# Optimization experiments

Measured on AMD Instinct MI355X. Metric: run time of the kernel, lower is better.

Reference implementation:

```python
import jax, jax.numpy as jnp
import numpy as np

EMB = 256
ENT_NUM = 100000
REL_NUM = 2000
B = 512


def setup_inputs() -> dict:
    key = jax.random.key(0)
    ks = jax.random.split(key, 10)
    s = 0.02
    return {
        "left_child": jax.random.normal(ks[0], (B, 3, EMB), jnp.float32),
        "right_child": jax.random.normal(ks[1], (B, 3, EMB), jnp.float32),
        "query": jax.random.normal(ks[2], (B, 3, EMB), jnp.float32),
        "ent_emb": jax.random.normal(ks[3], (ENT_NUM, EMB), jnp.float32) * s,
        "rel_emb": jax.random.normal(ks[4], (REL_NUM, EMB), jnp.float32) * s,
        "W_left": jax.random.normal(ks[5], (EMB, EMB), jnp.float32) * s,
        "b_left": jnp.zeros((EMB,), jnp.float32),
        "W_right": jax.random.normal(ks[6], (EMB, EMB), jnp.float32) * s,
        "b_right": jnp.zeros((EMB,), jnp.float32),
        "W_ent": jax.random.normal(ks[7], (EMB, 3 * EMB), jnp.float32) * s,
        "b_ent": jnp.zeros((EMB,), jnp.float32),
    }


def _attend(q, table):
    # q: [B, E], table: [N, E]. Fused form of expand*mul*sum + softmax + expand*mul*sum.
    logits = q @ table.T                     # [B, N]
    probs = jax.nn.softmax(logits, axis=1)   # [B, N]
    return probs @ table                     # [B, E]


def reference(left_child, right_child, query, ent_emb, rel_emb,
              W_left, b_left, W_right, b_right, W_ent, b_ent):
    q1 = query[:, 1, :]
    left_rel = q1 @ W_left.T + b_left
    right_rel = q1 @ W_right.T + b_right
    # cat(query[:,0], query[:,1], query[:,2]) along dim 1 == reshape
    q_cat = query.reshape(query.shape[0], 3 * EMB)
    q_ent = q_cat @ W_ent.T + b_ent

    o_ent = _attend(q_ent, ent_emb)
    o_left_r = _attend(left_rel, rel_emb)
    o_right_r = _attend(right_rel, rel_emb)

    new_left = jnp.stack([left_child[:, 0, :], o_left_r, o_ent], axis=1)
    new_right = jnp.stack([o_ent, o_right_r, right_child[:, 2, :]], axis=1)
    return (new_left, new_right)
```

## Files before the change

### kernel.cpp

```cpp
#include <hip/hip_runtime.h>
#include <hip/hip_bf16.h>
#include <math.h>

typedef __bf16 bf16;
typedef unsigned short u16;
typedef unsigned int u32;
typedef unsigned long long u64;
typedef long long i64;
typedef unsigned char u8;
typedef __attribute__((ext_vector_type(8))) __bf16 bf16x8;
typedef __attribute__((ext_vector_type(16))) float f32x16;
typedef __attribute__((ext_vector_type(8))) int i32x8;
typedef __attribute__((address_space(1))) void gvoid;
typedef __attribute__((address_space(3))) void svoid;

#define ENT_N 100000
#define REL_N 2000
#define ENT_CH 120
#define REL_CH 4

#define NPREPM 1536
#define NITEMS 6380
#define NCONVB 1792
#define NCOPY  256

static __device__ __forceinline__ i32x8 mk8(uint4 a, uint4 b) {
    i32x8 r;
    r[0] = (int)a.x; r[1] = (int)a.y; r[2] = (int)a.z; r[3] = (int)a.w;
    r[4] = (int)b.x; r[5] = (int)b.y; r[6] = (int)b.z; r[7] = (int)b.w;
    return r;
}

template<int KLEN>
static __device__ __forceinline__ void prep_tile(
    const float* __restrict__ query, const float* __restrict__ W,
    const float* __restrict__ bias, int b0, int rowbase, int qwoff,
    bf16* __restrict__ outBf, u8* __restrict__ out8, float* smem)
{
    const int t = threadIdx.x;
    float* qs = smem;
    float* Wl = smem + 4 * KLEN;

#pragma unroll
    for (int i = 0; i < 4 * KLEN / 256; ++i) {
        const int l = t + 256 * i;
        const int r = l / KLEN, k = l % KLEN;
        qs[l] = query[(size_t)(b0 + r) * 768 + qwoff + k];
    }

    const int j = t & 63, r = t >> 6;
    float acc = 0.f;
    const float* wbase = W + (size_t)rowbase * KLEN;

    for (int c = 0; c < KLEN / 32; ++c) {
        __syncthreads();
#pragma unroll
        for (int p = 0; p < 2; ++p) {
            const int idx = t + p * 256;
            const int row = idx >> 3, kq = idx & 7;
            const float4 v = *(const float4*)(wbase + (size_t)row * KLEN + c * 32 + kq * 4);
            float* d = Wl + row * 33 + kq * 4;
            d[0] = v.x; d[1] = v.y; d[2] = v.z; d[3] = v.w;
        }
        __syncthreads();
        const float* wr = Wl + j * 33;
        const float* qr = qs + r * KLEN + c * 32;
#pragma unroll
        for (int k = 0; k < 32; ++k) acc += wr[k] * qr[k];
    }
    acc += bias[rowbase + j];

    const size_t o = (size_t)(b0 + r) * 256 + rowbase + j;
    outBf[o] = (bf16)acc;
    out8[o] = (u8)__builtin_amdgcn_cvt_pk_fp8_f32(acc, acc, 0, false);
}

__global__ __launch_bounds__(256) void prep_conv(
    const float* __restrict__ query,
    const float* __restrict__ W_left, const float* __restrict__ b_left,
    const float* __restrict__ W_right, const float* __restrict__ b_right,
    const float* __restrict__ W_ent, const float* __restrict__ b_ent,
    const float* __restrict__ lc, const float* __restrict__ rc,
    bf16* __restrict__ qe, bf16* __restrict__ ql, bf16* __restrict__ qr,
    u8* __restrict__ qe8, u8* __restrict__ ql8, u8* __restrict__ qr8,
    float* __restrict__ out,
    const float* __restrict__ entF, const float* __restrict__ relF,
    u8* __restrict__ entT, u8* __restrict__ entB,
    u8* __restrict__ relT, u8* __restrict__ relB,
    int nconv)
{
    __shared__ float smem[5184];
    const int blk = blockIdx.x;
    const int t = threadIdx.x;

    if (blk >= nconv && blk < nconv + NPREPM) {
        const int pb = blk - nconv;
        const int rg = pb / 12, jt = pb % 12;
        const int b0 = rg * 4;
        const int proj = jt >> 2, rowbase = (jt & 3) * 64;
        if (proj == 0)
            prep_tile<768>(query, W_ent, b_ent, b0, rowbase, 0, qe, qe8, smem);
        else if (proj == 1)
            prep_tile<256>(query, W_left, b_left, b0, rowbase, 256, ql, ql8, smem);
        else
            prep_tile<256>(query, W_right, b_right, b0, rowbase, 256, qr, qr8, smem);
        return;
    }
    if (blk >= nconv + NPREPM) {
        const int idx = (blk - nconv - NPREPM) * 256 + t;
        if (idx < 32768) {
            const int q = idx >> 6, e4 = idx & 63;
            float4 v = *(const float4*)(lc + (size_t)q * 768 + e4 * 4);
            *(float4*)(out + (size_t)q * 768 + e4 * 4) = v;
        } else {
            const int j = idx - 32768;
            const int q = j >> 6, e4 = j & 63;
            float4 v = *(const float4*)(rc + (size_t)q * 768 + 512 + e4 * 4);
            *(float4*)(out + (size_t)393216 + q * 768 + 512 + e4 * 4) = v;
        }
        return;
    }

    float* tile = smem;
    const int eg = t & 7, rowb = t >> 3;

    float4 A0, B0, A1, B1;

    auto cissue = [&](int it) {
        const int x = it >> 2, y = it & 3;
        const float* in; int R, g;
        if (x < 1563) { in = entF; R = ENT_N; g = x; }
        else          { in = relF; R = REL_N; g = x - 1563; }
        const int r0 = g * 64, e0 = y * 64;
        const int ra = r0 + rowb, rb = r0 + rowb + 32;
        if (ra < R) {
            const float* s0 = in + (size_t)ra * 256 + e0 + eg * 8;
            A0 = *(const float4*)s0; B0 = *(const float4*)(s0 + 4);
        } else { A0 = make_float4(0.f, 0.f, 0.f, 0.f); B0 = A0; }
        if (rb < R) {
            const float* s1 = in + (size_t)rb * 256 + e0 + eg * 8;
            A1 = *(const float4*)s1; B1 = *(const float4*)(s1 + 4);
        } else { A1 = make_float4(0.f, 0.f, 0.f, 0.f); B1 = A1; }
    };

    auto cemit = [&](int it) {
        const int x = it >> 2, y = it & 3;
        u8* oT; u8* oB; int g;
        if (x < 1563) { oT = entT; oB = entB; g = x; }
        else          { oT = relT; oB = relB; g = x - 1563; }
        {
            const int n2 = t >> 2, piece = t & 3;
            const int sub = n2 >> 5, nn = n2 & 31;
            const int kbk = piece >> 1, jh = piece & 1;
            const float* src = tile + n2 * 65 + kbk * 32 + jh * 16;
            u32 xx; uint4 o;
            xx = __builtin_amdgcn_cvt_pk_fp8_f32(src[0], src[1], 0, false);
            o.x = __builtin_amdgcn_cvt_pk_fp8_f32(src[2], src[3], xx, true);
            xx = __builtin_amdgcn_cvt_pk_fp8_f32(src[4], src[5], 0, false);
            o.y = __builtin_amdgcn_cvt_pk_fp8_f32(src[6], src[7], xx, true);
            xx = __builtin_amdgcn_cvt_pk_fp8_f32(src[8], src[9], 0, false);
            o.z = __builtin_amdgcn_cvt_pk_fp8_f32(src[10], src[11], xx, true);
            xx = __builtin_amdgcn_cvt_pk_fp8_f32(src[12], src[13], 0, false);
            o.w = __builtin_amdgcn_cvt_pk_fp8_f32(src[14], src[15], xx, true);
            *(uint4*)(oB + (size_t)g * 16384 + sub * 8192 +
                      (size_t)y * 2048 + kbk * 1024 + nn * 32 + jh * 16) = o;
        }
        {
            const int etl = t >> 7, kbv = (t >> 6) & 1;
            const int nv = (t >> 1) & 31, jh = t & 1;
            const int colL = etl * 32 + nv;
            float v[16];
#pragma unroll
            for (int i = 0; i < 16; ++i) {
                const int row = jh * 32 + (i & 3) + 8 * (i >> 2) + 4 * kbv;
                v[i] = tile[row * 65 + colL];
            }
            u32 xx; uint4 o;
            xx = __builtin_amdgcn_cvt_pk_fp8_f32(v[0], v[1], 0, false);
            o.x = __builtin_amdgcn_cvt_pk_fp8_f32(v[2], v[3], xx, true);
            xx = __builtin_amdgcn_cvt_pk_fp8_f32(v[4], v[5], 0, false);
            o.y = __builtin_amdgcn_cvt_pk_fp8_f32(v[6], v[7], xx, true);
            xx = __builtin_amdgcn_cvt_pk_fp8_f32(v[8], v[9], 0, false);
            o.z = __builtin_amdgcn_cvt_pk_fp8_f32(v[10], v[11], xx, true);
            xx = __builtin_amdgcn_cvt_pk_fp8_f32(v[12], v[13], 0, false);
            o.w = __builtin_amdgcn_cvt_pk_fp8_f32(v[14], v[15], xx, true);
            *(uint4*)(oT + (size_t)g * 16384 +
                      (size_t)(y * 2 + etl) * 2048 +
                      kbv * 1024 + nv * 32 + jh * 16) = o;
        }
    };

    int it = blk;
    cissue(it);
    while (it < NITEMS) {
        const int nxt = it + NCONVB;
        __syncthreads();
        {
            float* d0 = tile + rowb * 65 + eg * 8;
            d0[0] = A0.x; d0[1] = A0.y; d0[2] = A0.z; d0[3] = A0.w;
            d0[4] = B0.x; d0[5] = B0.y; d0[6] = B0.z; d0[7] = B0.w;
            float* d1 = tile + (rowb + 32) * 65 + eg * 8;
            d1[0] = A1.x; d1[1] = A1.y; d1[2] = A1.z; d1[3] = A1.w;
            d1[4] = B1.x; d1[5] = B1.y; d1[6] = B1.z; d1[7] = B1.w;
        }
        if (nxt < NITEMS) cissue(nxt);
        __syncthreads();
        cemit(it);
        it = nxt;
    }
}

__global__ __launch_bounds__(256, 2) void flash10(
    const u8* __restrict__ qeP, const u8* __restrict__ qlP,
    const u8* __restrict__ qrP,
    const u8* __restrict__ entB, const u8* __restrict__ relB,
    const u8* __restrict__ entT, const u8* __restrict__ relT,
    float* __restrict__ entL, float* __restrict__ relLL,
    float* __restrict__ relLR,
    u16* __restrict__ entO, u16* __restrict__ relOL, u16* __restrict__ relOR)
{
    const int tid = threadIdx.x;
    const int w = tid >> 6;
    const int lane = tid & 63;
    const int n = lane & 31;
    const int kb = lane >> 5;

    int qt, c, stride, nt, Nrows;
    const u8* qbf; const u8* tabB; const u8* tabT;
    float* pL; u16* pO;
    {
        const int id = blockIdx.x;
        if (id < 480) {
            qt = id / 120; c = id % 120;
            stride = 120; nt = (c < 3) ? 14 : 13;
            Nrows = ENT_N;
            qbf = qeP; tabB = entB; tabT = entT; pL = entL; pO = entO;
        } else {
            const int r = id - 480;
            qt = (r >> 2) & 3; c = r & 3;
            stride = 4; nt = 8;
            Nrows = REL_N;
            tabB = relB; tabT = relT;
            if (r < 16) { qbf = qlP; pL = relLL; pO = relOL; }
            else        { qbf = qrP; pL = relLR; pO = relOR; }
        }
    }
    const int q0 = qt * 128;
    const int qw = q0 + w * 32;

    __shared__ __align__(16) u8 lds[65536];
    u16* lds16 = (u16*)lds;

    const u8* qrow = qbf + (size_t)(qw + n) * 256;
    i32x8 qf[4];
#pragma unroll
    for (int kc = 0; kc < 4; ++kc) {
        uint4 a = *(const uint4*)(qrow + kc * 64 + kb * 32);
        uint4 b = *(const uint4*)(qrow + kc * 64 + kb * 32 + 16);
        qf[kc] = mk8(a, b);
    }

    f32x16 acc[8];
#pragma unroll
    for (int et = 0; et < 8; ++et)
#pragma unroll
        for (int i = 0; i < 16; ++i) acc[et][i] = 0.f;
    float l_run = 0.f;

    auto stage = [&](int buf, int g) {
        u8* sK = lds + buf * 32768;
        u8* sV = sK + 16384;
        const u8* ksrc = tabB + (size_t)g * 16384 + w * 4096 + (size_t)lane * 16;
        const u8* vsrc = tabT + (size_t)g * 16384 + w * 4096 + (size_t)lane * 16;
#pragma unroll
        for (int o = 0; o < 4096; o += 1024) {
            __builtin_amdgcn_global_load_lds((gvoid*)(ksrc + o),
                                             (svoid*)(sK + w * 4096 + o), 16, 0, 0);
            __builtin_amdgcn_global_load_lds((gvoid*)(vsrc + o),
                                             (svoid*)(sV + w * 4096 + o), 16, 0, 0);
        }
    };

    int rt = c;
    stage(0, rt);
    __syncthreads();

    for (int k = 0; k < nt; ++k) {
        if (k + 1 < nt) stage((k + 1) & 1, rt + stride);

        const u8* sK = lds + (k & 1) * 32768;
        const u8* sV = sK + 16384;
        const int gr = rt * 64;

        f32x16 L0, L1;
#pragma unroll
        for (int i = 0; i < 16; ++i) { L0[i] = 0.f; L1[i] = 0.f; }
        const u8* kbase = sK + kb * 1024 + n * 32;
#pragma unroll
        for (int kc = 0; kc < 4; ++kc) {
            uint4 a0 = *(const uint4*)(kbase + kc * 2048);
            uint4 a1 = *(const uint4*)(kbase + kc * 2048 + 16);
            L0 = __builtin_amdgcn_mfma_scale_f32_32x32x64_f8f6f4(
                mk8(a0, a1), qf[kc], L0, 0, 0, 0, 0x7f7f7f7f, 0, 0x7f7f7f7f);
            uint4 b0 = *(const uint4*)(kbase + 8192 + kc * 2048);
            uint4 b1 = *(const uint4*)(kbase + 8192 + kc * 2048 + 16);
            L1 = __builtin_amdgcn_mfma_scale_f32_32x32x64_f8f6f4(
                mk8(b0, b1), qf[kc], L1, 0, 0, 0, 0x7f7f7f7f, 0, 0x7f7f7f7f);
        }
        if (gr + 64 > Nrows) {
#pragma unroll
            for (int r = 0; r < 16; ++r) {
                const int row = (r & 3) + 8 * (r >> 2) + 4 * kb;
                if (gr + row >= Nrows)      L0[r] = -1e30f;
                if (gr + 32 + row >= Nrows) L1[r] = -1e30f;
            }
        }
        float rs = 0.f;
#pragma unroll
        for (int r = 0; r < 16; ++r) {
            const float p0 = __expf(L0[r]); L0[r] = p0; rs += p0;
            const float p1 = __expf(L1[r]); L1[r] = p1; rs += p1;
        }
        rs += __shfl_xor(rs, 32);
        l_run += rs;
        u32 p[8];
#pragma unroll
        for (int i = 0; i < 4; ++i) {
            u32 x = __builtin_amdgcn_cvt_pk_fp8_f32(L0[i * 4 + 0], L0[i * 4 + 1], 0, false);
            p[i] = __builtin_amdgcn_cvt_pk_fp8_f32(L0[i * 4 + 2], L0[i * 4 + 3], x, true);
            u32 y = __builtin_amdgcn_cvt_pk_fp8_f32(L1[i * 4 + 0], L1[i * 4 + 1], 0, false);
            p[i + 4] = __builtin_amdgcn_cvt_pk_fp8_f32(L1[i * 4 + 2], L1[i * 4 + 3], y, true);
        }
        uint4 pa; pa.x = p[0]; pa.y = p[1]; pa.z = p[2]; pa.w = p[3];
        uint4 pb; pb.x = p[4]; pb.y = p[5]; pb.z = p[6]; pb.w = p[7];
        const i32x8 bv = mk8(pa, pb);
        const u8* vbase = sV + kb * 1024 + n * 32;
#pragma unroll
        for (int et = 0; et < 8; ++et) {
            uint4 v0 = *(const uint4*)(vbase + et * 2048);
            uint4 v1 = *(const uint4*)(vbase + et * 2048 + 16);
            acc[et] = __builtin_amdgcn_mfma_scale_f32_32x32x64_f8f6f4(
                mk8(v0, v1), bv, acc[et], 0, 0, 0, 0x7f7f7f7f, 0, 0x7f7f7f7f);
        }
        rt += stride;
        __syncthreads();
    }

    if (lane < 32) pL[(size_t)c * 512 + qw + n] = l_run;

    for (int half = 0; half < 2; ++half) {
        __syncthreads();
        if ((w >> 1) == half) {
            u16* rgn = lds16 + (w & 1) * 8448;
#pragma unroll
            for (int et = 0; et < 8; ++et)
#pragma unroll
                for (int a2 = 0; a2 < 4; ++a2) {
                    bf16 h0 = (bf16)acc[et][a2 * 4 + 0];
                    bf16 h1 = (bf16)acc[et][a2 * 4 + 1];
                    bf16 h2 = (bf16)acc[et][a2 * 4 + 2];
                    bf16 h3 = (bf16)acc[et][a2 * 4 + 3];
                    uint2 pk;
                    pk.x = ((u32)(*(u16*)&h1) << 16) | (u32)(*(u16*)&h0);
                    pk.y = ((u32)(*(u16*)&h3) << 16) | (u32)(*(u16*)&h2);
                    *(uint2*)(rgn + n * 264 + et * 32 + 8 * a2 + 4 * kb) = pk;
                }
        }
        __syncthreads();
#pragma unroll
        for (int rg = 0; rg < 2; ++rg) {
            const int qt2 = q0 + (half * 2 + rg) * 32;
            const u16* src = lds16 + rg * 8448;
            const int qq = tid >> 3, e0 = (tid & 7) * 32;
#pragma unroll
            for (int i = 0; i < 4; ++i) {
                const u16* sp = src + qq * 264 + e0 + i * 8;
                uint2 a = *(const uint2*)(sp);
                uint2 b = *(const uint2*)(sp + 4);
                uint4 wv; wv.x = a.x; wv.y = a.y; wv.z = b.x; wv.w = b.y;
                *(uint4*)(pO + ((size_t)c * 512 + qt2 + qq) * 256 + e0 + i * 8) = wv;
            }
        }
    }
}

__global__ __launch_bounds__(256) void combine_all(
    const u16* __restrict__ entO, const float* __restrict__ entL,
    const u16* __restrict__ relOL, const float* __restrict__ relLL,
    const u16* __restrict__ relOR, const float* __restrict__ relLR,
    float* __restrict__ out)
{
    const u16* pO; const float* pl; int CH, baseA, baseB;
    if (blockIdx.y == 0) { pO = entO; pl = entL; CH = ENT_CH; baseA = 512; baseB = 393216; }
    else if (blockIdx.y == 1) { pO = relOL; pl = relLL; CH = REL_CH; baseA = 256; baseB = -1; }
    else { pO = relOR; pl = relLR; CH = REL_CH; baseA = 393472; baseB = -1; }

    const int t = threadIdx.x;
    const int qi = t >> 7;
    const int e0g = (t >> 2) & 31;
    const int seg = t & 3;
    const int q = blockIdx.x * 2 + qi;
    const int e0 = e0g * 8;
    const int cnt = CH >> 2;
    const int cbeg = seg * cnt;

    float s = 0.f;
    float a[8];
#pragma unroll
    for (int k = 0; k < 8; ++k) a[k] = 0.f;
#pragma unroll 6
    for (int c = cbeg; c < cbeg + cnt; ++c) {
        s += pl[(size_t)c * 512 + q];
        const uint4 wv = *(const uint4*)(pO + ((size_t)c * 512 + q) * 256 + e0);
        const u32 ww[4] = {wv.x, wv.y, wv.z, wv.w};
#pragma unroll
        for (int p = 0; p < 4; ++p) {
            a[p * 2]     += __uint_as_float((ww[p] & 0xffffu) << 16);
            a[p * 2 + 1] += __uint_as_float(ww[p] & 0xffff0000u);
        }
    }

    __shared__ float red[2][32][4][11];
    float* slot = red[qi][e0g][seg];
#pragma unroll
    for (int k = 0; k < 8; ++k) slot[k] = a[k];
    slot[8] = s;
    __syncthreads();
    if (seg == 0) {
        float st = 0.f;
        float b[8];
#pragma unroll
        for (int k = 0; k < 8; ++k) b[k] = 0.f;
#pragma unroll
        for (int sgi = 0; sgi < 4; ++sgi) {
            const float* sl = red[qi][e0g][sgi];
            st += sl[8];
#pragma unroll
            for (int k = 0; k < 8; ++k) b[k] += sl[k];
        }
        const float inv = 1.f / st;
#pragma unroll
        for (int k = 0; k < 8; ++k) b[k] *= inv;
        float4 o1 = {b[0], b[1], b[2], b[3]};
        float4 o2 = {b[4], b[5], b[6], b[7]};
        *(float4*)(out + (size_t)baseA + (size_t)q * 768 + e0) = o1;
        *(float4*)(out + (size_t)baseA + (size_t)q * 768 + e0 + 4) = o2;
        if (baseB >= 0) {
            *(float4*)(out + (size_t)baseB + (size_t)q * 768 + e0) = o1;
            *(float4*)(out + (size_t)baseB + (size_t)q * 768 + e0 + 4) = o2;
        }
    }
}

__global__ __launch_bounds__(256) void attend_simple(
    const bf16* __restrict__ qbf, const float* __restrict__ tab, int Nrows,
    float* __restrict__ out, int baseA, int baseB)
{
    const int q = blockIdx.x;
    const int t = threadIdx.x, wave = t >> 6, lane = t & 63;
    float qv[4];
#pragma unroll
    for (int i = 0; i < 4; ++i) qv[i] = (float)qbf[(size_t)q * 256 + lane + 64 * i];
    float m = -INFINITY, l = 0.f, o[4] = {0.f, 0.f, 0.f, 0.f};
    for (int r = wave; r < Nrows; r += 4) {
        const float* row = tab + (size_t)r * 256;
        float d = 0.f;
#pragma unroll
        for (int i = 0; i < 4; ++i) d += qv[i] * row[lane + 64 * i];
#pragma unroll
        for (int s = 32; s; s >>= 1) d += __shfl_xor(d, s);
        const float mn = fmaxf(m, d);
        const float al = __expf(m - mn);
        const float p = __expf(d - mn);
#pragma unroll
        for (int i = 0; i < 4; ++i) o[i] = o[i] * al + p * row[lane + 64 * i];
        l = l * al + p; m = mn;
    }
    __shared__ float sm[4], sl[4], so[4][256];
    if (lane == 0) { sm[wave] = m; sl[wave] = l; }
#pragma unroll
    for (int i = 0; i < 4; ++i) so[wave][lane + 64 * i] = o[i];
    __syncthreads();
    const float M = fmaxf(fmaxf(sm[0], sm[1]), fmaxf(sm[2], sm[3]));
    const float w0 = __expf(sm[0] - M), w1 = __expf(sm[1] - M);
    const float w2 = __expf(sm[2] - M), w3 = __expf(sm[3] - M);
    const float L = w0 * sl[0] + w1 * sl[1] + w2 * sl[2] + w3 * sl[3];
    const float a = (w0 * so[0][t] + w1 * so[1][t] + w2 * so[2][t] + w3 * so[3][t]) / L;
    out[(size_t)baseA + (size_t)q * 768 + t] = a;
    if (baseB >= 0) out[(size_t)baseB + (size_t)q * 768 + t] = a;
}

extern "C" void kernel_launch(void* const* d_in, const int* in_sizes, int n_in,
                              void* d_out, int out_size, void* d_ws, size_t ws_size,
                              hipStream_t stream)
{
    const float* left_child  = (const float*)d_in[0];
    const float* right_child = (const float*)d_in[1];
    const float* query       = (const float*)d_in[2];
    const float* ent_emb     = (const float*)d_in[3];
    const float* rel_emb     = (const float*)d_in[4];
    const float* W_left      = (const float*)d_in[5];
    const float* b_left      = (const float*)d_in[6];
    const float* W_right     = (const float*)d_in[7];
    const float* b_right     = (const float*)d_in[8];
    const float* W_ent       = (const float*)d_in[9];
    const float* b_ent       = (const float*)d_in[10];
    float* out = (float*)d_out;
    char* ws = (char*)d_ws;

    bf16* qe_bf = (bf16*)(ws + 0);
    bf16* ql_bf = (bf16*)(ws + 262144);
    bf16* qr_bf = (bf16*)(ws + 524288);
    u8*   qe8   = (u8*)(ws + 786432);
    u8*   ql8   = (u8*)(ws + 917504);
    u8*   qr8   = (u8*)(ws + 1048576);
    u8*   entT8 = (u8*)(ws + 1179648);
    u8*   relT8 = (u8*)(ws + 26787840);
    u8*   entB8 = (u8*)(ws + 27312128);
    u8*   relB8 = (u8*)(ws + 52920320);
    float* entL = (float*)(ws + 53444608);
    u16*  entO  = (u16*)(ws + 53690368);
    float* relLL = (float*)(ws + 85147648);
    float* relLR = (float*)(ws + 85155840);
    u16*  relOL = (u16*)(ws + 85164032);
    u16*  relOR = (u16*)(ws + 86212608);
    const size_t WS_FULL = 87261184;
    const size_t WS_FALLBACK = 786432;

    if (ws_size >= WS_FULL) {
        prep_conv<<<dim3(NCONVB + NPREPM + NCOPY), dim3(256), 0, stream>>>(
            query, W_left, b_left, W_right, b_right, W_ent, b_ent,
            left_child, right_child, qe_bf, ql_bf, qr_bf, qe8, ql8, qr8, out,
            ent_emb, rel_emb, entT8, entB8, relT8, relB8, NCONVB);
        flash10<<<dim3(512), dim3(256), 0, stream>>>(
            qe8, ql8, qr8, entB8, relB8, entT8, relT8,
            entL, relLL, relLR, entO, relOL, relOR);
        combine_all<<<dim3(256, 3), dim3(256), 0, stream>>>(
            entO, entL, relOL, relLL, relOR, relLR, out);
    } else if (ws_size >= WS_FALLBACK) {
        prep_conv<<<dim3(NPREPM + NCOPY), dim3(256), 0, stream>>>(
            query, W_left, b_left, W_right, b_right, W_ent, b_ent,
            left_child, right_child, qe_bf, ql_bf, qr_bf, qe8, ql8, qr8, out,
            ent_emb, rel_emb, (u8*)ws, (u8*)ws, (u8*)ws, (u8*)ws, 0);
        attend_simple<<<dim3(512), dim3(256), 0, stream>>>(qe_bf, ent_emb, ENT_N, out, 512, 393216);
        attend_simple<<<dim3(512), dim3(256), 0, stream>>>(ql_bf, rel_emb, REL_N, out, 256, -1);
        attend_simple<<<dim3(512), dim3(256), 0, stream>>>(qr_bf, rel_emb, REL_N, out, 393472, -1);
    }
    (void)in_sizes; (void)n_in; (void)out_size;
}
```

Baseline: 252.1 us.

## Fuse prep, flash attention and combine into one persistent kernel with grid barriers

Replaces the three launches (prep/convert, flash attention, combine) with one persistent kernel of 512 blocks. The stages are separated by atomic-counter grid barriers, and the table conversion loop prefetches the next item's loads. It also double-buffers the weight tiles in the projection prep. This removes launch gaps and tail idle time between kernels, at the cost of a memset, spin-wait barriers that rely on all 512 blocks being co-resident, and lower per-stage occupancy flexibility.

```diff
diff --git a/kernel.cpp b/kernel.cpp
--- a/kernel.cpp
+++ b/kernel.cpp
@@ -8,7 +8,6 @@
 typedef unsigned long long u64;
 typedef long long i64;
 typedef unsigned char u8;
-typedef __attribute__((ext_vector_type(8))) __bf16 bf16x8;
 typedef __attribute__((ext_vector_type(16))) float f32x16;
 typedef __attribute__((ext_vector_type(8))) int i32x8;
 typedef __attribute__((address_space(1))) void gvoid;
@@ -21,14 +20,26 @@
 
 #define NPREPM 1536
 #define NITEMS 6380
-#define NCONVB 1792
 #define NCOPY  256
+#define NBLK   512
 
 static __device__ __forceinline__ i32x8 mk8(uint4 a, uint4 b) {
     i32x8 r;
     r[0] = (int)a.x; r[1] = (int)a.y; r[2] = (int)a.z; r[3] = (int)a.w;
     r[4] = (int)b.x; r[5] = (int)b.y; r[6] = (int)b.z; r[7] = (int)b.w;
     return r;
+}
+
+static __device__ __forceinline__ void grid_barrier(u32* cnt) {
+    __syncthreads();
+    if (threadIdx.x == 0) {
+        __threadfence();
+        atomicAdd(cnt, 1u);
+        while (atomicAdd(cnt, 0u) < (u32)NBLK)
+            __builtin_amdgcn_s_sleep(2);
+        __threadfence();
+    }
+    __syncthreads();
 }
 
 template<int KLEN>
@@ -49,24 +60,33 @@
     }
 
     const int j = t & 63, r = t >> 6;
+    const int srow = t >> 3, skq = t & 7;
+    const float* wbase = W + (size_t)rowbase * KLEN;
+
+    float4 v0, v1;
+    auto wload = [&](int c) {
+        v0 = *(const float4*)(wbase + (size_t)srow * KLEN + c * 32 + skq * 4);
+        v1 = *(const float4*)(wbase + (size_t)(srow + 32) * KLEN + c * 32 + skq * 4);
+    };
+    auto wstore = [&](float* dst) {
+        float* d0 = dst + srow * 33 + skq * 4;
+        d0[0] = v0.x; d0[1] = v0.y; d0[2] = v0.z; d0[3] = v0.w;
+        float* d1 = dst + (srow + 32) * 33 + skq * 4;
+        d1[0] = v1.x; d1[1] = v1.y; d1[2] = v1.z; d1[3] = v1.w;
+    };
+
     float acc = 0.f;
-    const float* wbase = W + (size_t)rowbase * KLEN;
-
-    for (int c = 0; c < KLEN / 32; ++c) {
+    wload(0);
+    wstore(Wl);
+    constexpr int NC = KLEN / 32;
+    for (int c = 0; c < NC; ++c) {
+        if (c + 1 < NC) wload(c + 1);
         __syncthreads();
-#pragma unroll
-        for (int p = 0; p < 2; ++p) {
-            const int idx = t + p * 256;
-            const int row = idx >> 3, kq = idx & 7;
-            const float4 v = *(const float4*)(wbase + (size_t)row * KLEN + c * 32 + kq * 4);
-            float* d = Wl + row * 33 + kq * 4;
-            d[0] = v.x; d[1] = v.y; d[2] = v.z; d[3] = v.w;
-        }
-        __syncthreads();
-        const float* wr = Wl + j * 33;
+        const float* wr = Wl + (c & 1) * 2112 + j * 33;
         const float* qr = qs + r * KLEN + c * 32;
 #pragma unroll
         for (int k = 0; k < 32; ++k) acc += wr[k] * qr[k];
+        if (c + 1 < NC) wstore(Wl + ((c + 1) & 1) * 2112);
     }
     acc += bias[rowbase + j];
 
@@ -75,7 +95,372 @@
     out8[o] = (u8)__builtin_amdgcn_cvt_pk_fp8_f32(acc, acc, 0, false);
 }
 
-__global__ __launch_bounds__(256) void prep_conv(
+struct FusedArgs {
+    const float *query, *W_left, *b_left, *W_right, *b_right, *W_ent, *b_ent;
+    const float *lc, *rc, *entF, *relF;
+    bf16 *qe, *ql, *qr;
+    u8 *qe8, *ql8, *qr8;
+    u8 *entT, *entB, *relT, *relB;
+    float *entL, *relLL, *relLR;
+    u16 *entO, *relOL, *relOR;
+    float *out;
+    u32 *cnt0, *cnt1;
+};
+
+__global__ __launch_bounds__(256, 2) void fused_all(FusedArgs A)
+{
+    const int t = threadIdx.x;
+    const int tid = t;
+    const int w = tid >> 6;
+    const int lane = tid & 63;
+    const int n = lane & 31;
+    const int kb = lane >> 5;
+
+    __shared__ __align__(16) u8 lds[65536];
+
+    {
+        float* tile = (float*)lds;
+        const int eg = t & 7, rowb = t >> 3;
+        float4 A0, B0, A1, B1;
+        int pf = -1;
+
+        auto cissue = [&](int it) {
+            const int x = it >> 2, y = it & 3;
+            const float* in; int R, g;
+            if (x < 1563) { in = A.entF; R = ENT_N; g = x; }
+            else          { in = A.relF; R = REL_N; g = x - 1563; }
+            const int r0 = g * 64, e0 = y * 64;
+            const int ra = r0 + rowb, rb = r0 + rowb + 32;
+            if (ra < R) {
+                const float* s0 = in + (size_t)ra * 256 + e0 + eg * 8;
+                A0 = *(const float4*)s0; B0 = *(const float4*)(s0 + 4);
+            } else { A0 = make_float4(0.f, 0.f, 0.f, 0.f); B0 = A0; }
+            if (rb < R) {
+                const float* s1 = in + (size_t)rb * 256 + e0 + eg * 8;
+                A1 = *(const float4*)s1; B1 = *(const float4*)(s1 + 4);
+            } else { A1 = make_float4(0.f, 0.f, 0.f, 0.f); B1 = A1; }
+        };
+        auto cemit = [&](int it) {
+            const int x = it >> 2, y = it & 3;
+            u8* oT; u8* oB; int g;
+            if (x < 1563) { oT = A.entT; oB = A.entB; g = x; }
+            else          { oT = A.relT; oB = A.relB; g = x - 1563; }
+            {
+                const int n2 = t >> 2, piece = t & 3;
+                const int sub = n2 >> 5, nn = n2 & 31;
+                const int kbk = piece >> 1, jh = piece & 1;
+                const float* src = tile + n2 * 65 + kbk * 32 + jh * 16;
+                u32 xx; uint4 o;
+                xx = __builtin_amdgcn_cvt_pk_fp8_f32(src[0], src[1], 0, false);
+                o.x = __builtin_amdgcn_cvt_pk_fp8_f32(src[2], src[3], xx, true);
+                xx = __builtin_amdgcn_cvt_pk_fp8_f32(src[4], src[5], 0, false);
+                o.y = __builtin_amdgcn_cvt_pk_fp8_f32(src[6], src[7], xx, true);
+                xx = __builtin_amdgcn_cvt_pk_fp8_f32(src[8], src[9], 0, false);
+                o.z = __builtin_amdgcn_cvt_pk_fp8_f32(src[10], src[11], xx, true);
+                xx = __builtin_amdgcn_cvt_pk_fp8_f32(src[12], src[13], 0, false);
+                o.w = __builtin_amdgcn_cvt_pk_fp8_f32(src[14], src[15], xx, true);
+                *(uint4*)(oB + (size_t)g * 16384 + sub * 8192 +
+                          (size_t)y * 2048 + kbk * 1024 + nn * 32 + jh * 16) = o;
+            }
+            {
+                const int etl = t >> 7, kbv = (t >> 6) & 1;
+                const int nv = (t >> 1) & 31, jh = t & 1;
+                const int colL = etl * 32 + nv;
+                float v[16];
+#pragma unroll
+                for (int i = 0; i < 16; ++i) {
+                    const int row = jh * 32 + (i & 3) + 8 * (i >> 2) + 4 * kbv;
+                    v[i] = tile[row * 65 + colL];
+                }
+                u32 xx; uint4 o;
+                xx = __builtin_amdgcn_cvt_pk_fp8_f32(v[0], v[1], 0, false);
+                o.x = __builtin_amdgcn_cvt_pk_fp8_f32(v[2], v[3], xx, true);
+                xx = __builtin_amdgcn_cvt_pk_fp8_f32(v[4], v[5], 0, false);
+                o.y = __builtin_amdgcn_cvt_pk_fp8_f32(v[6], v[7], xx, true);
+                xx = __builtin_amdgcn_cvt_pk_fp8_f32(v[8], v[9], 0, false);
+                o.z = __builtin_amdgcn_cvt_pk_fp8_f32(v[10], v[11], xx, true);
+                xx = __builtin_amdgcn_cvt_pk_fp8_f32(v[12], v[13], 0, false);
+                o.w = __builtin_amdgcn_cvt_pk_fp8_f32(v[14], v[15], xx, true);
+                *(uint4*)(oT + (size_t)g * 16384 +
+                          (size_t)(y * 2 + etl) * 2048 +
+                          kbv * 1024 + nv * 32 + jh * 16) = o;
+            }
+        };
+
+        for (int it = blockIdx.x; it < NITEMS + NPREPM + NCOPY; it += NBLK) {
+            if (it < NITEMS) {
+                if (pf != it) cissue(it);
+                __syncthreads();
+                float* d0 = tile + rowb * 65 + eg * 8;
+                d0[0] = A0.x; d0[1] = A0.y; d0[2] = A0.z; d0[3] = A0.w;
+                d0[4] = B0.x; d0[5] = B0.y; d0[6] = B0.z; d0[7] = B0.w;
+                float* d1 = tile + (rowb + 32) * 65 + eg * 8;
+                d1[0] = A1.x; d1[1] = A1.y; d1[2] = A1.z; d1[3] = A1.w;
+                d1[4] = B1.x; d1[5] = B1.y; d1[6] = B1.z; d1[7] = B1.w;
+                const int nxt = it + NBLK;
+                if (nxt < NITEMS) { cissue(nxt); pf = nxt; }
+                __syncthreads();
+                cemit(it);
+            } else if (it < NITEMS + NPREPM) {
+                __syncthreads();
+                const int pb = it - NITEMS;
+                const int rg = pb / 12, jt = pb % 12;
+                const int b0 = rg * 4;
+                const int proj = jt >> 2, rowbase = (jt & 3) * 64;
+                if (proj == 0)
+                    prep_tile<768>(A.query, A.W_ent, A.b_ent, b0, rowbase, 0,
+                                   A.qe, A.qe8, (float*)lds);
+                else if (proj == 1)
+                    prep_tile<256>(A.query, A.W_left, A.b_left, b0, rowbase, 256,
+                                   A.ql, A.ql8, (float*)lds);
+                else
+                    prep_tile<256>(A.query, A.W_right, A.b_right, b0, rowbase, 256,
+                                   A.qr, A.qr8, (float*)lds);
+            } else {
+                const int idx = (it - NITEMS - NPREPM) * 256 + t;
+                if (idx < 32768) {
+                    const int q = idx >> 6, e4 = idx & 63;
+                    float4 v = *(const float4*)(A.lc + (size_t)q * 768 + e4 * 4);
+                    *(float4*)(A.out + (size_t)q * 768 + e4 * 4) = v;
+                } else {
+                    const int j2 = idx - 32768;
+                    const int q = j2 >> 6, e4 = j2 & 63;
+                    float4 v = *(const float4*)(A.rc + (size_t)q * 768 + 512 + e4 * 4);
+                    *(float4*)(A.out + (size_t)393216 + q * 768 + 512 + e4 * 4) = v;
+                }
+            }
+        }
+    }
+    grid_barrier(A.cnt0);
+
+    {
+        u16* lds16 = (u16*)lds;
+        int qt, c, stride, nt, Nrows;
+        const u8* qbf; const u8* tabB; const u8* tabT;
+        float* pL; u16* pO;
+        {
+            const int id = blockIdx.x;
+            if (id < 480) {
+                qt = id / 120; c = id % 120;
+                stride = 120; nt = (c < 3) ? 14 : 13;
+                Nrows = ENT_N;
+                qbf = A.qe8; tabB = A.entB; tabT = A.entT; pL = A.entL; pO = A.entO;
+            } else {
+                const int r = id - 480;
+                qt = (r >> 2) & 3; c = r & 3;
+                stride = 4; nt = 8;
+                Nrows = REL_N;
+                tabB = A.relB; tabT = A.relT;
+                if (r < 16) { qbf = A.ql8; pL = A.relLL; pO = A.relOL; }
+                else        { qbf = A.qr8; pL = A.relLR; pO = A.relOR; }
+            }
+        }
+        const int q0 = qt * 128;
+        const int qw = q0 + w * 32;
+
+        const u8* qrow = qbf + (size_t)(qw + n) * 256;
+        i32x8 qf[4];
+#pragma unroll
+        for (int kc = 0; kc < 4; ++kc) {
+            uint4 a = *(const uint4*)(qrow + kc * 64 + kb * 32);
+            uint4 b = *(const uint4*)(qrow + kc * 64 + kb * 32 + 16);
+            qf[kc] = mk8(a, b);
+        }
+
+        f32x16 acc[8];
+#pragma unroll
+        for (int et = 0; et < 8; ++et)
+#pragma unroll
+            for (int i = 0; i < 16; ++i) acc[et][i] = 0.f;
+        float l_run = 0.f;
+
+        auto stage = [&](int buf, int g2) {
+            u8* sK = lds + buf * 32768;
+            u8* sV = sK + 16384;
+            const u8* ksrc = tabB + (size_t)g2 * 16384 + w * 4096 + (size_t)lane * 16;
+            const u8* vsrc = tabT + (size_t)g2 * 16384 + w * 4096 + (size_t)lane * 16;
+#pragma unroll
+            for (int o = 0; o < 4096; o += 1024) {
+                __builtin_amdgcn_global_load_lds((gvoid*)(ksrc + o),
+                                                 (svoid*)(sK + w * 4096 + o), 16, 0, 0);
+                __builtin_amdgcn_global_load_lds((gvoid*)(vsrc + o),
+                                                 (svoid*)(sV + w * 4096 + o), 16, 0, 0);
+            }
+        };
+
+        int rt = c;
+        stage(0, rt);
+        __syncthreads();
+
+        for (int k = 0; k < nt; ++k) {
+            if (k + 1 < nt) stage((k + 1) & 1, rt + stride);
+
+            const u8* sK = lds + (k & 1) * 32768;
+            const u8* sV = sK + 16384;
+            const int gr = rt * 64;
+
+            f32x16 L0, L1;
+#pragma unroll
+            for (int i = 0; i < 16; ++i) { L0[i] = 0.f; L1[i] = 0.f; }
+            const u8* kbase = sK + kb * 1024 + n * 32;
+#pragma unroll
+            for (int kc = 0; kc < 4; ++kc) {
+                uint4 a0 = *(const uint4*)(kbase + kc * 2048);
+                uint4 a1 = *(const uint4*)(kbase + kc * 2048 + 16);
+                L0 = __builtin_amdgcn_mfma_scale_f32_32x32x64_f8f6f4(
+                    mk8(a0, a1), qf[kc], L0, 0, 0, 0, 0x7f7f7f7f, 0, 0x7f7f7f7f);
+                uint4 b0 = *(const uint4*)(kbase + 8192 + kc * 2048);
+                uint4 b1 = *(const uint4*)(kbase + 8192 + kc * 2048 + 16);
+                L1 = __builtin_amdgcn_mfma_scale_f32_32x32x64_f8f6f4(
+                    mk8(b0, b1), qf[kc], L1, 0, 0, 0, 0x7f7f7f7f, 0, 0x7f7f7f7f);
+            }
+            if (gr + 64 > Nrows) {
+#pragma unroll
+                for (int r = 0; r < 16; ++r) {
+                    const int row = (r & 3) + 8 * (r >> 2) + 4 * kb;
+                    if (gr + row >= Nrows)      L0[r] = -1e30f;
+                    if (gr + 32 + row >= Nrows) L1[r] = -1e30f;
+                }
+            }
+            float rs = 0.f;
+#pragma unroll
+            for (int r = 0; r < 16; ++r) {
+                const float p0 = __expf(L0[r]); L0[r] = p0; rs += p0;
+                const float p1 = __expf(L1[r]); L1[r] = p1; rs += p1;
+            }
+            rs += __shfl_xor(rs, 32);
+            l_run += rs;
+            u32 p[8];
+#pragma unroll
+            for (int i = 0; i < 4; ++i) {
+                u32 x = __builtin_amdgcn_cvt_pk_fp8_f32(L0[i * 4 + 0], L0[i * 4 + 1], 0, false);
+                p[i] = __builtin_amdgcn_cvt_pk_fp8_f32(L0[i * 4 + 2], L0[i * 4 + 3], x, true);
+                u32 y = __builtin_amdgcn_cvt_pk_fp8_f32(L1[i * 4 + 0], L1[i * 4 + 1], 0, false);
+                p[i + 4] = __builtin_amdgcn_cvt_pk_fp8_f32(L1[i * 4 + 2], L1[i * 4 + 3], y, true);
+            }
+            uint4 pa; pa.x = p[0]; pa.y = p[1]; pa.z = p[2]; pa.w = p[3];
+            uint4 pb; pb.x = p[4]; pb.y = p[5]; pb.z = p[6]; pb.w = p[7];
+            const i32x8 bv = mk8(pa, pb);
+            const u8* vbase = sV + kb * 1024 + n * 32;
+#pragma unroll
+            for (int et = 0; et < 8; ++et) {
+                uint4 v0 = *(const uint4*)(vbase + et * 2048);
+                uint4 v1 = *(const uint4*)(vbase + et * 2048 + 16);
+                acc[et] = __builtin_amdgcn_mfma_scale_f32_32x32x64_f8f6f4(
+                    mk8(v0, v1), bv, acc[et], 0, 0, 0, 0x7f7f7f7f, 0, 0x7f7f7f7f);
+            }
+            rt += stride;
+            __syncthreads();
+        }
+
+        if (lane < 32) pL[(size_t)c * 512 + qw + n] = l_run;
+
+        for (int half = 0; half < 2; ++half) {
+            __syncthreads();
+            if ((w >> 1) == half) {
+                u16* rgn = lds16 + (w & 1) * 8448;
+#pragma unroll
+                for (int et = 0; et < 8; ++et)
+#pragma unroll
+                    for (int a2 = 0; a2 < 4; ++a2) {
+                        bf16 h0 = (bf16)acc[et][a2 * 4 + 0];
+                        bf16 h1 = (bf16)acc[et][a2 * 4 + 1];
+                        bf16 h2 = (bf16)acc[et][a2 * 4 + 2];
+                        bf16 h3 = (bf16)acc[et][a2 * 4 + 3];
+                        uint2 pk;
+                        pk.x = ((u32)(*(u16*)&h1) << 16) | (u32)(*(u16*)&h0);
+                        pk.y = ((u32)(*(u16*)&h3) << 16) | (u32)(*(u16*)&h2);
+                        *(uint2*)(rgn + n * 264 + et * 32 + 8 * a2 + 4 * kb) = pk;
+                    }
+            }
+            __syncthreads();
+#pragma unroll
+            for (int rg = 0; rg < 2; ++rg) {
+                const int qt2 = q0 + (half * 2 + rg) * 32;
+                const u16* src = lds16 + rg * 8448;
+                const int qq = tid >> 3, e0 = (tid & 7) * 32;
+#pragma unroll
+                for (int i = 0; i < 4; ++i) {
+                    const u16* sp = src + qq * 264 + e0 + i * 8;
+                    uint2 a = *(const uint2*)(sp);
+                    uint2 b = *(const uint2*)(sp + 4);
+                    uint4 wv; wv.x = a.x; wv.y = a.y; wv.z = b.x; wv.w = b.y;
+                    *(uint4*)(pO + ((size_t)c * 512 + qt2 + qq) * 256 + e0 + i * 8) = wv;
+                }
+            }
+        }
+    }
+    grid_barrier(A.cnt1);
+
+    {
+        typedef float RedT[32][4][11];
+        RedT* red = (RedT*)lds;
+        for (int v = blockIdx.x; v < 768; v += NBLK) {
+            __syncthreads();
+            const int gx = v & 255, gy = v >> 8;
+            const u16* pO; const float* pl; int CH, baseA, baseB;
+            if (gy == 0) { pO = A.entO; pl = A.entL; CH = ENT_CH; baseA = 512; baseB = 393216; }
+            else if (gy == 1) { pO = A.relOL; pl = A.relLL; CH = REL_CH; baseA = 256; baseB = -1; }
+            else { pO = A.relOR; pl = A.relLR; CH = REL_CH; baseA = 393472; baseB = -1; }
+
+            const int qi = t >> 7;
+            const int e0g = (t >> 2) & 31;
+            const int seg = t & 3;
+            const int q = gx * 2 + qi;
+            const int e0 = e0g * 8;
+            const int cnt = CH >> 2;
+            const int cbeg = seg * cnt;
+
+            float s = 0.f;
+            float a[8];
+#pragma unroll
+            for (int k = 0; k < 8; ++k) a[k] = 0.f;
+#pragma unroll 6
+            for (int c = cbeg; c < cbeg + cnt; ++c) {
+                s += pl[(size_t)c * 512 + q];
+                const uint4 wv = *(const uint4*)(pO + ((size_t)c * 512 + q) * 256 + e0);
+                const u32 ww[4] = {wv.x, wv.y, wv.z, wv.w};
+#pragma unroll
+                for (int p = 0; p < 4; ++p) {
+                    a[p * 2]     += __uint_as_float((ww[p] & 0xffffu) << 16);
+                    a[p * 2 + 1] += __uint_as_float(ww[p] & 0xffff0000u);
+                }
+            }
+
+            float* slot = red[qi][e0g][seg];
+#pragma unroll
+            for (int k = 0; k < 8; ++k) slot[k] = a[k];
+            slot[8] = s;
+            __syncthreads();
+            if (seg == 0) {
+                float st = 0.f;
+                float b[8];
+#pragma unroll
+                for (int k = 0; k < 8; ++k) b[k] = 0.f;
+#pragma unroll
+                for (int sgi = 0; sgi < 4; ++sgi) {
+                    const float* sl = red[qi][e0g][sgi];
+                    st += sl[8];
+#pragma unroll
+                    for (int k = 0; k < 8; ++k) b[k] += sl[k];
+                }
+                const float inv = 1.f / st;
+#pragma unroll
+                for (int k = 0; k < 8; ++k) b[k] *= inv;
+                float4 o1 = {b[0], b[1], b[2], b[3]};
+                float4 o2 = {b[4], b[5], b[6], b[7]};
+                *(float4*)(A.out + (size_t)baseA + (size_t)q * 768 + e0) = o1;
+                *(float4*)(A.out + (size_t)baseA + (size_t)q * 768 + e0 + 4) = o2;
+                if (baseB >= 0) {
+                    *(float4*)(A.out + (size_t)baseB + (size_t)q * 768 + e0) = o1;
+                    *(float4*)(A.out + (size_t)baseB + (size_t)q * 768 + e0 + 4) = o2;
+                }
+            }
+        }
+    }
+}
+
+__global__ __launch_bounds__(256) void prep_copy(
     const float* __restrict__ query,
     const float* __restrict__ W_left, const float* __restrict__ b_left,
     const float* __restrict__ W_right, const float* __restrict__ b_right,
@@ -83,19 +468,14 @@
     const float* __restrict__ lc, const float* __restrict__ rc,
     bf16* __restrict__ qe, bf16* __restrict__ ql, bf16* __restrict__ qr,
     u8* __restrict__ qe8, u8* __restrict__ ql8, u8* __restrict__ qr8,
-    float* __restrict__ out,
-    const float* __restrict__ entF, const float* __restrict__ relF,
-    u8* __restrict__ entT, u8* __restrict__ entB,
-    u8* __restrict__ relT, u8* __restrict__ relB,
-    int nconv)
+    float* __restrict__ out)
 {
-    __shared__ float smem[5184];
+    __shared__ float smem[7296];
     const int blk = blockIdx.x;
     const int t = threadIdx.x;
 
-    if (blk >= nconv && blk < nconv + NPREPM) {
-        const int pb = blk - nconv;
-        const int rg = pb / 12, jt = pb % 12;
+    if (blk < NPREPM) {
+        const int rg = blk / 12, jt = blk % 12;
         const int b0 = rg * 4;
         const int proj = jt >> 2, rowbase = (jt & 3) * 64;
         if (proj == 0)
@@ -106,349 +486,16 @@
             prep_tile<256>(query, W_right, b_right, b0, rowbase, 256, qr, qr8, smem);
         return;
     }
-    if (blk >= nconv + NPREPM) {
-        const int idx = (blk - nconv - NPREPM) * 256 + t;
-        if (idx < 32768) {
-            const int q = idx >> 6, e4 = idx & 63;
-            float4 v = *(const float4*)(lc + (size_t)q * 768 + e4 * 4);
-            *(float4*)(out + (size_t)q * 768 + e4 * 4) = v;
-        } else {
-            const int j = idx - 32768;
-            const int q = j >> 6, e4 = j & 63;
-            float4 v = *(const float4*)(rc + (size_t)q * 768 + 512 + e4 * 4);
-            *(float4*)(out + (size_t)393216 + q * 768 + 512 + e4 * 4) = v;
-        }
-        return;
-    }
-
-    float* tile = smem;
-    const int eg = t & 7, rowb = t >> 3;
-
-    float4 A0, B0, A1, B1;
-
-    auto cissue = [&](int it) {
-        const int x = it >> 2, y = it & 3;
-        const float* in; int R, g;
-        if (x < 1563) { in = entF; R = ENT_N; g = x; }
-        else          { in = relF; R = REL_N; g = x - 1563; }
-        const int r0 = g * 64, e0 = y * 64;
-        const int ra = r0 + rowb, rb = r0 + rowb + 32;
-        if (ra < R) {
-            const float* s0 = in + (size_t)ra * 256 + e0 + eg * 8;
-            A0 = *(const float4*)s0; B0 = *(const float4*)(s0 + 4);
-        } else { A0 = make_float4(0.f, 0.f, 0.f, 0.f); B0 = A0; }
-        if (rb < R) {
-            const float* s1 = in + (size_t)rb * 256 + e0 + eg * 8;
-            A1 = *(const float4*)s1; B1 = *(const float4*)(s1 + 4);
-        } else { A1 = make_float4(0.f, 0.f, 0.f, 0.f); B1 = A1; }
-    };
-
-    auto cemit = [&](int it) {
-        const int x = it >> 2, y = it & 3;
-        u8* oT; u8* oB; int g;
-        if (x < 1563) { oT = entT; oB = entB; g = x; }
-        else          { oT = relT; oB = relB; g = x - 1563; }
-        {
-            const int n2 = t >> 2, piece = t & 3;
-            const int sub = n2 >> 5, nn = n2 & 31;
-            const int kbk = piece >> 1, jh = piece & 1;
-            const float* src = tile + n2 * 65 + kbk * 32 + jh * 16;
-            u32 xx; uint4 o;
-            xx = __builtin_amdgcn_cvt_pk_fp8_f32(src[0], src[1], 0, false);
-            o.x = __builtin_amdgcn_cvt_pk_fp8_f32(src[2], src[3], xx, true);
-            xx = __builtin_amdgcn_cvt_pk_fp8_f32(src[4], src[5], 0, false);
-            o.y = __builtin_amdgcn_cvt_pk_fp8_f32(src[6], src[7], xx, true);
-            xx = __builtin_amdgcn_cvt_pk_fp8_f32(src[8], src[9], 0, false);
-            o.z = __builtin_amdgcn_cvt_pk_fp8_f32(src[10], src[11], xx, true);
-            xx = __builtin_amdgcn_cvt_pk_fp8_f32(src[12], src[13], 0, false);
-            o.w = __builtin_amdgcn_cvt_pk_fp8_f32(src[14], src[15], xx, true);
-            *(uint4*)(oB + (size_t)g * 16384 + sub * 8192 +
-                      (size_t)y * 2048 + kbk * 1024 + nn * 32 + jh * 16) = o;
-        }
-        {
-            const int etl = t >> 7, kbv = (t >> 6) & 1;
-            const int nv = (t >> 1) & 31, jh = t & 1;
-            const int colL = etl * 32 + nv;
-            float v[16];
-#pragma unroll
-            for (int i = 0; i < 16; ++i) {
-                const int row = jh * 32 + (i & 3) + 8 * (i >> 2) + 4 * kbv;
-                v[i] = tile[row * 65 + colL];
-            }
-            u32 xx; uint4 o;
-            xx = __builtin_amdgcn_cvt_pk_fp8_f32(v[0], v[1], 0, false);
-            o.x = __builtin_amdgcn_cvt_pk_fp8_f32(v[2], v[3], xx, true);
-            xx = __builtin_amdgcn_cvt_pk_fp8_f32(v[4], v[5], 0, false);
-            o.y = __builtin_amdgcn_cvt_pk_fp8_f32(v[6], v[7], xx, true);
-            xx = __builtin_amdgcn_cvt_pk_fp8_f32(v[8], v[9], 0, false);
-            o.z = __builtin_amdgcn_cvt_pk_fp8_f32(v[10], v[11], xx, true);
-            xx = __builtin_amdgcn_cvt_pk_fp8_f32(v[12], v[13], 0, false);
-            o.w = __builtin_amdgcn_cvt_pk_fp8_f32(v[14], v[15], xx, true);
-            *(uint4*)(oT + (size_t)g * 16384 +
-                      (size_t)(y * 2 + etl) * 2048 +
-                      kbv * 1024 + nv * 32 + jh * 16) = o;
-        }
-    };
-
-    int it = blk;
-    cissue(it);
-    while (it < NITEMS) {
-        const int nxt = it + NCONVB;
-        __syncthreads();
-        {
-            float* d0 = tile + rowb * 65 + eg * 8;
-            d0[0] = A0.x; d0[1] = A0.y; d0[2] = A0.z; d0[3] = A0.w;
-            d0[4] = B0.x; d0[5] = B0.y; d0[6] = B0.z; d0[7] = B0.w;
-            float* d1 = tile + (rowb + 32) * 65 + eg * 8;
-            d1[0] = A1.x; d1[1] = A1.y; d1[2] = A1.z; d1[3] = A1.w;
-            d1[4] = B1.x; d1[5] = B1.y; d1[6] = B1.z; d1[7] = B1.w;
-        }
-        if (nxt < NITEMS) cissue(nxt);
-        __syncthreads();
-        cemit(it);
-        it = nxt;
-    }
-}
-
-__global__ __launch_bounds__(256, 2) void flash10(
-    const u8* __restrict__ qeP, const u8* __restrict__ qlP,
-    const u8* __restrict__ qrP,
-    const u8* __restrict__ entB, const u8* __restrict__ relB,
-    const u8* __restrict__ entT, const u8* __restrict__ relT,
-    float* __restrict__ entL, float* __restrict__ relLL,
-    float* __restrict__ relLR,
-    u16* __restrict__ entO, u16* __restrict__ relOL, u16* __restrict__ relOR)
-{
-    const int tid = threadIdx.x;
-    const int w = tid >> 6;
-    const int lane = tid & 63;
-    const int n = lane & 31;
-    const int kb = lane >> 5;
-
-    int qt, c, stride, nt, Nrows;
-    const u8* qbf; const u8* tabB; const u8* tabT;
-    float* pL; u16* pO;
-    {
-        const int id = blockIdx.x;
-        if (id < 480) {
-            qt = id / 120; c = id % 120;
-            stride = 120; nt = (c < 3) ? 14 : 13;
-            Nrows = ENT_N;
-            qbf = qeP; tabB = entB; tabT = entT; pL = entL; pO = entO;
-        } else {
-            const int r = id - 480;
-            qt = (r >> 2) & 3; c = r & 3;
-            stride = 4; nt = 8;
-            Nrows = REL_N;
-            tabB = relB; tabT = relT;
-            if (r < 16) { qbf = qlP; pL = relLL; pO = relOL; }
-            else        { qbf = qrP; pL = relLR; pO = relOR; }
-        }
-    }
-    const int q0 = qt * 128;
-    const int qw = q0 + w * 32;
-
-    __shared__ __align__(16) u8 lds[65536];
-    u16* lds16 = (u16*)lds;
-
-    const u8* qrow = qbf + (size_t)(qw + n) * 256;
-    i32x8 qf[4];
-#pragma unroll
-    for (int kc = 0; kc < 4; ++kc) {
-        uint4 a = *(const uint4*)(qrow + kc * 64 + kb * 32);
-        uint4 b = *(const uint4*)(qrow + kc * 64 + kb * 32 + 16);
-        qf[kc] = mk8(a, b);
-    }
-
-    f32x16 acc[8];
-#pragma unroll
-    for (int et = 0; et < 8; ++et)
-#pragma unroll
-        for (int i = 0; i < 16; ++i) acc[et][i] = 0.f;
-    float l_run = 0.f;
-
-    auto stage = [&](int buf, int g) {
-        u8* sK = lds + buf * 32768;
-        u8* sV = sK + 16384;
-        const u8* ksrc = tabB + (size_t)g * 16384 + w * 4096 + (size_t)lane * 16;
-        const u8* vsrc = tabT + (size_t)g * 16384 + w * 4096 + (size_t)lane * 16;
-#pragma unroll
-        for (int o = 0; o < 4096; o += 1024) {
-            __builtin_amdgcn_global_load_lds((gvoid*)(ksrc + o),
-                                             (svoid*)(sK + w * 4096 + o), 16, 0, 0);
-            __builtin_amdgcn_global_load_lds((gvoid*)(vsrc + o),
-                                             (svoid*)(sV + w * 4096 + o), 16, 0, 0);
-        }
-    };
-
-    int rt = c;
-    stage(0, rt);
-    __syncthreads();
-
-    for (int k = 0; k < nt; ++k) {
-        if (k + 1 < nt) stage((k + 1) & 1, rt + stride);
-
-        const u8* sK = lds + (k & 1) * 32768;
-        const u8* sV = sK + 16384;
-        const int gr = rt * 64;
-
-        f32x16 L0, L1;
-#pragma unroll
-        for (int i = 0; i < 16; ++i) { L0[i] = 0.f; L1[i] = 0.f; }
-        const u8* kbase = sK + kb * 1024 + n * 32;
-#pragma unroll
-        for (int kc = 0; kc < 4; ++kc) {
-            uint4 a0 = *(const uint4*)(kbase + kc * 2048);
-            uint4 a1 = *(const uint4*)(kbase + kc * 2048 + 16);
-            L0 = __builtin_amdgcn_mfma_scale_f32_32x32x64_f8f6f4(
-                mk8(a0, a1), qf[kc], L0, 0, 0, 0, 0x7f7f7f7f, 0, 0x7f7f7f7f);
-            uint4 b0 = *(const uint4*)(kbase + 8192 + kc * 2048);
-            uint4 b1 = *(const uint4*)(kbase + 8192 + kc * 2048 + 16);
-            L1 = __builtin_amdgcn_mfma_scale_f32_32x32x64_f8f6f4(
-                mk8(b0, b1), qf[kc], L1, 0, 0, 0, 0x7f7f7f7f, 0, 0x7f7f7f7f);
-        }
-        if (gr + 64 > Nrows) {
-#pragma unroll
-            for (int r = 0; r < 16; ++r) {
-                const int row = (r & 3) + 8 * (r >> 2) + 4 * kb;
-                if (gr + row >= Nrows)      L0[r] = -1e30f;
-                if (gr + 32 + row >= Nrows) L1[r] = -1e30f;
-            }
-        }
-        float rs = 0.f;
-#pragma unroll
-        for (int r = 0; r < 16; ++r) {
-            const float p0 = __expf(L0[r]); L0[r] = p0; rs += p0;
-            const float p1 = __expf(L1[r]); L1[r] = p1; rs += p1;
-        }
-        rs += __shfl_xor(rs, 32);
-        l_run += rs;
-        u32 p[8];
-#pragma unroll
-        for (int i = 0; i < 4; ++i) {
-            u32 x = __builtin_amdgcn_cvt_pk_fp8_f32(L0[i * 4 + 0], L0[i * 4 + 1], 0, false);
-            p[i] = __builtin_amdgcn_cvt_pk_fp8_f32(L0[i * 4 + 2], L0[i * 4 + 3], x, true);
-            u32 y = __builtin_amdgcn_cvt_pk_fp8_f32(L1[i * 4 + 0], L1[i * 4 + 1], 0, false);
-            p[i + 4] = __builtin_amdgcn_cvt_pk_fp8_f32(L1[i * 4 + 2], L1[i * 4 + 3], y, true);
-        }
-        uint4 pa; pa.x = p[0]; pa.y = p[1]; pa.z = p[2]; pa.w = p[3];
-        uint4 pb; pb.x = p[4]; pb.y = p[5]; pb.z = p[6]; pb.w = p[7];
-        const i32x8 bv = mk8(pa, pb);
-        const u8* vbase = sV + kb * 1024 + n * 32;
-#pragma unroll
-        for (int et = 0; et < 8; ++et) {
-            uint4 v0 = *(const uint4*)(vbase + et * 2048);
-            uint4 v1 = *(const uint4*)(vbase + et * 2048 + 16);
-            acc[et] = __builtin_amdgcn_mfma_scale_f32_32x32x64_f8f6f4(
-                mk8(v0, v1), bv, acc[et], 0, 0, 0, 0x7f7f7f7f, 0, 0x7f7f7f7f);
-        }
-        rt += stride;
-        __syncthreads();
-    }
-
-    if (lane < 32) pL[(size_t)c * 512 + qw + n] = l_run;
-
-    for (int half = 0; half < 2; ++half) {
-        __syncthreads();
-        if ((w >> 1) == half) {
-            u16* rgn = lds16 + (w & 1) * 8448;
-#pragma unroll
-            for (int et = 0; et < 8; ++et)
-#pragma unroll
-                for (int a2 = 0; a2 < 4; ++a2) {
-                    bf16 h0 = (bf16)acc[et][a2 * 4 + 0];
-                    bf16 h1 = (bf16)acc[et][a2 * 4 + 1];
-                    bf16 h2 = (bf16)acc[et][a2 * 4 + 2];
-                    bf16 h3 = (bf16)acc[et][a2 * 4 + 3];
-                    uint2 pk;
-                    pk.x = ((u32)(*(u16*)&h1) << 16) | (u32)(*(u16*)&h0);
-                    pk.y = ((u32)(*(u16*)&h3) << 16) | (u32)(*(u16*)&h2);
-                    *(uint2*)(rgn + n * 264 + et * 32 + 8 * a2 + 4 * kb) = pk;
-                }
-        }
-        __syncthreads();
-#pragma unroll
-        for (int rg = 0; rg < 2; ++rg) {
-            const int qt2 = q0 + (half * 2 + rg) * 32;
-            const u16* src = lds16 + rg * 8448;
-            const int qq = tid >> 3, e0 = (tid & 7) * 32;
-#pragma unroll
-            for (int i = 0; i < 4; ++i) {
-                const u16* sp = src + qq * 264 + e0 + i * 8;
-                uint2 a = *(const uint2*)(sp);
-                uint2 b = *(const uint2*)(sp + 4);
-                uint4 wv; wv.x = a.x; wv.y = a.y; wv.z = b.x; wv.w = b.y;
-                *(uint4*)(pO + ((size_t)c * 512 + qt2 + qq) * 256 + e0 + i * 8) = wv;
-            }
-        }
-    }
-}
-
-__global__ __launch_bounds__(256) void combine_all(
-    const u16* __restrict__ entO, const float* __restrict__ entL,
-    const u16* __restrict__ relOL, const float* __restrict__ relLL,
-    const u16* __restrict__ relOR, const float* __restrict__ relLR,
-    float* __restrict__ out)
-{
-    const u16* pO; const float* pl; int CH, baseA, baseB;
-    if (blockIdx.y == 0) { pO = entO; pl = entL; CH = ENT_CH; baseA = 512; baseB = 393216; }
-    else if (blockIdx.y == 1) { pO = relOL; pl = relLL; CH = REL_CH; baseA = 256; baseB = -1; }
-    else { pO = relOR; pl = relLR; CH = REL_CH; baseA = 393472; baseB = -1; }
-
-    const int t = threadIdx.x;
-    const int qi = t >> 7;
-    const int e0g = (t >> 2) & 31;
-    const int seg = t & 3;
-    const int q = blockIdx.x * 2 + qi;
-    const int e0 = e0g * 8;
-    const int cnt = CH >> 2;
-    const int cbeg = seg * cnt;
-
-    float s = 0.f;
-    float a[8];
-#pragma unroll
-    for (int k = 0; k < 8; ++k) a[k] = 0.f;
-#pragma unroll 6
-    for (int c = cbeg; c < cbeg + cnt; ++c) {
-        s += pl[(size_t)c * 512 + q];
-        const uint4 wv = *(const uint4*)(pO + ((size_t)c * 512 + q) * 256 + e0);
-        const u32 ww[4] = {wv.x, wv.y, wv.z, wv.w};
-#pragma unroll
-        for (int p = 0; p < 4; ++p) {
-            a[p * 2]     += __uint_as_float((ww[p] & 0xffffu) << 16);
-            a[p * 2 + 1] += __uint_as_float(ww[p] & 0xffff0000u);
-        }
-    }
-
-    __shared__ float red[2][32][4][11];
-    float* slot = red[qi][e0g][seg];
-#pragma unroll
-    for (int k = 0; k < 8; ++k) slot[k] = a[k];
-    slot[8] = s;
-    __syncthreads();
-    if (seg == 0) {
-        float st = 0.f;
-        float b[8];
-#pragma unroll
-        for (int k = 0; k < 8; ++k) b[k] = 0.f;
-#pragma unroll
-        for (int sgi = 0; sgi < 4; ++sgi) {
-            const float* sl = red[qi][e0g][sgi];
-            st += sl[8];
-#pragma unroll
-            for (int k = 0; k < 8; ++k) b[k] += sl[k];
-        }
-        const float inv = 1.f / st;
-#pragma unroll
-        for (int k = 0; k < 8; ++k) b[k] *= inv;
-        float4 o1 = {b[0], b[1], b[2], b[3]};
-        float4 o2 = {b[4], b[5], b[6], b[7]};
-        *(float4*)(out + (size_t)baseA + (size_t)q * 768 + e0) = o1;
-        *(float4*)(out + (size_t)baseA + (size_t)q * 768 + e0 + 4) = o2;
-        if (baseB >= 0) {
-            *(float4*)(out + (size_t)baseB + (size_t)q * 768 + e0) = o1;
-            *(float4*)(out + (size_t)baseB + (size_t)q * 768 + e0 + 4) = o2;
-        }
+    const int idx = (blk - NPREPM) * 256 + t;
+    if (idx < 32768) {
+        const int q = idx >> 6, e4 = idx & 63;
+        float4 v = *(const float4*)(lc + (size_t)q * 768 + e4 * 4);
+        *(float4*)(out + (size_t)q * 768 + e4 * 4) = v;
+    } else {
+        const int j = idx - 32768;
+        const int q = j >> 6, e4 = j & 63;
+        float4 v = *(const float4*)(rc + (size_t)q * 768 + 512 + e4 * 4);
+        *(float4*)(out + (size_t)393216 + q * 768 + 512 + e4 * 4) = v;
     }
 }
 
@@ -524,24 +571,30 @@
     float* relLR = (float*)(ws + 85155840);
     u16*  relOL = (u16*)(ws + 85164032);
     u16*  relOR = (u16*)(ws + 86212608);
-    const size_t WS_FULL = 87261184;
+    u32*  cnts  = (u32*)(ws + 87261184);
+    const size_t WS_FULL = 87261440;
     const size_t WS_FALLBACK = 786432;
 
     if (ws_size >= WS_FULL) {
-        prep_conv<<<dim3(NCONVB + NPREPM + NCOPY), dim3(256), 0, stream>>>(
+        hipMemsetAsync((void*)cnts, 0, 256, stream);
+        FusedArgs ha;
+        ha.query = query; ha.W_left = W_left; ha.b_left = b_left;
+        ha.W_right = W_right; ha.b_right = b_right;
+        ha.W_ent = W_ent; ha.b_ent = b_ent;
+        ha.lc = left_child; ha.rc = right_child;
+        ha.entF = ent_emb; ha.relF = rel_emb;
+        ha.qe = qe_bf; ha.ql = ql_bf; ha.qr = qr_bf;
+        ha.qe8 = qe8; ha.ql8 = ql8; ha.qr8 = qr8;
+        ha.entT = entT8; ha.entB = entB8; ha.relT = relT8; ha.relB = relB8;
+        ha.entL = entL; ha.relLL = relLL; ha.relLR = relLR;
+        ha.entO = entO; ha.relOL = relOL; ha.relOR = relOR;
+        ha.out = out;
+        ha.cnt0 = cnts; ha.cnt1 = cnts + 16;
+        fused_all<<<dim3(NBLK), dim3(256), 0, stream>>>(ha);
+    } else if (ws_size >= WS_FALLBACK) {
+        prep_copy<<<dim3(NPREPM + NCOPY), dim3(256), 0, stream>>>(
             query, W_left, b_left, W_right, b_right, W_ent, b_ent,
-            left_child, right_child, qe_bf, ql_bf, qr_bf, qe8, ql8, qr8, out,
-            ent_emb, rel_emb, entT8, entB8, relT8, relB8, NCONVB);
-        flash10<<<dim3(512), dim3(256), 0, stream>>>(
-            qe8, ql8, qr8, entB8, relB8, entT8, relT8,
-            entL, relLL, relLR, entO, relOL, relOR);
-        combine_all<<<dim3(256, 3), dim3(256), 0, stream>>>(
-            entO, entL, relOL, relLL, relOR, relLR, out);
-    } else if (ws_size >= WS_FALLBACK) {
-        prep_conv<<<dim3(NPREPM + NCOPY), dim3(256), 0, stream>>>(
-            query, W_left, b_left, W_right, b_right, W_ent, b_ent,
-            left_child, right_child, qe_bf, ql_bf, qr_bf, qe8, ql8, qr8, out,
-            ent_emb, rel_emb, (u8*)ws, (u8*)ws, (u8*)ws, (u8*)ws, 0);
+            left_child, right_child, qe_bf, ql_bf, qr_bf, qe8, ql8, qr8, out);
         attend_simple<<<dim3(512), dim3(256), 0, stream>>>(qe_bf, ent_emb, ENT_N, out, 512, 393216);
         attend_simple<<<dim3(512), dim3(256), 0, stream>>>(ql_bf, rel_emb, REL_N, out, 256, -1);
         attend_simple<<<dim3(512), dim3(256), 0, stream>>>(qr_bf, rel_emb, REL_N, out, 393472, -1);
```

Measured after the change: 378.9 us. 50.3% more time.
